# Kernel optimization log

Measured on AMD Instinct MI355X. Metric: run time of the kernel, lower is better.

## Reference

```python
import jax, jax.numpy as jnp
import numpy as np

B, SZ_C, S, D_KV, H_DIM = 2048, 8, 32, 32, 512
NEG = B // 4  # batchsize > 64 branch
TEMP = 0.5
EPS = 1e-8
BN_EPS = 1e-5


def setup_inputs() -> dict:
    key = jax.random.key(0)
    ks = jax.random.split(key, 8)
    x = jax.random.normal(ks[0], (B, SZ_C, S, D_KV), dtype=jnp.float32)
    W1 = jax.random.normal(ks[1], (H_DIM, D_KV), dtype=jnp.float32) * 0.05
    b1 = jnp.zeros((H_DIM,), jnp.float32)
    gamma = jnp.ones((H_DIM,), jnp.float32)
    beta = jnp.zeros((H_DIM,), jnp.float32)
    W2 = jax.random.normal(ks[2], (D_KV, H_DIM), dtype=jnp.float32) * 0.05
    b2 = jnp.zeros((D_KV,), jnp.float32)
    fcW = jax.random.normal(ks[3], (32, S * D_KV), dtype=jnp.float32) * 0.03
    fcb = jnp.zeros((32,), jnp.float32)
    # negatives: raw draws in [0, B-1); shifted past the self index inside reference
    neg_idx = jax.random.randint(ks[4], (B, NEG), 0, B - 1, dtype=jnp.int32)
    return {"x": x, "W1": W1, "b1": b1, "gamma": gamma, "beta": beta,
            "W2": W2, "b2": b2, "fcW": fcW, "fcb": fcb, "neg_idx": neg_idx}


def reference(x, W1, b1, gamma, beta, W2, b2, fcW, fcb, neg_idx):
    # per-channel MLP with training-mode BatchNorm (stats over the B*S rows of each channel)
    xc = jnp.transpose(x, (1, 0, 2, 3)).reshape(SZ_C, B * S, D_KV)   # [C, N, d_kv]
    h = jnp.einsum('cnd,hd->cnh', xc, W1) + b1                        # [C, N, h]
    mu = jnp.mean(h, axis=1, keepdims=True)
    var = jnp.mean((h - mu) ** 2, axis=1, keepdims=True)              # biased, as BN
    h = jax.nn.relu((h - mu) * jax.lax.rsqrt(var + BN_EPS) * gamma + beta)
    y = jnp.einsum('cnh,dh->cnd', h, W2) + b2                         # [C, N, d_kv]
    y = y.reshape(SZ_C, B, S * D_KV)                                  # raw flatten == torch views
    Zc = jnp.einsum('cbf,of->cbo', y, fcW) + fcb                      # [C, B, 32]
    Z = jnp.transpose(Zc, (1, 0, 2))                                  # [B, C, 32]

    Zn = Z / jnp.clip(jnp.linalg.norm(Z, axis=-1, keepdims=True), EPS, None)

    # shift raw draws in [0, B-1) past i -> uniform over indices != i
    idx = neg_idx + (neg_idx >= jnp.arange(B, dtype=neg_idx.dtype)[:, None]).astype(neg_idx.dtype)
    neg = Zn[idx]                                                     # [B, NEG, C, 32]
    neg_sim = jnp.einsum('bcd,bncd->bn', Zn, neg) / SZ_C              # mean over channels

    # mean pairwise cosine similarity across channels (j < k)
    G = jnp.einsum('bjd,bkd->bjk', Zn, Zn)                            # [B, C, C]
    mask = jnp.triu(jnp.ones((SZ_C, SZ_C), bool), 1)
    num_comb = SZ_C * (SZ_C - 1) // 2
    pos_sim = jnp.where(mask, G, 0.0).sum(axis=(1, 2)) / num_comb     # [B]

    l = jnp.exp(pos_sim / TEMP) / jnp.sum(jnp.exp(neg_sim / TEMP), axis=1)  # [B]
    Z_out = jnp.mean(Z, axis=1)                                       # [B, 32]
    return Z_out, l
```

## Files before the change

### kernel.cpp

```cpp
#include <hip/hip_runtime.h>
#include <hip/hip_bf16.h>
#include <math.h>

#define NB 2048
#define NC 8
#define NNEG 512

typedef __attribute__((ext_vector_type(8))) short bf16x8;
typedef __attribute__((ext_vector_type(4))) float f32x4;
typedef __attribute__((ext_vector_type(16))) float f32x16;

static __device__ __forceinline__ unsigned short f2b(float f) {
  __hip_bfloat16 h = __float2bfloat16(f);
  return *reinterpret_cast<unsigned short*>(&h);
}
static __device__ __forceinline__ unsigned int packbf2(float a, float b) {
  return (unsigned int)f2b(a) | ((unsigned int)f2b(b) << 16);
}

#define WS_SSUM   0
#define WS_SPROD  256
#define WS_B1EFF  8448
#define WS_Z      12544
#define WS_POS    536832
#define WS_W1B    538880
#define WS_W2B    604416
#define WS_FCWB   612608
#define WS_ZNB    628992

__global__ __launch_bounds__(256) void k_stats(const float* __restrict__ x,
                        float* __restrict__ Ssum, float* __restrict__ Sprod) {
  int c = blockIdx.y;
  int t = threadIdx.x;
  int w = t >> 6, l = t & 63;
  int col = l & 31, half = l >> 5;
  f32x16 acc;
  #pragma unroll
  for (int r = 0; r < 16; ++r) acc[r] = 0.f;
  float ssum = 0.f;
  #pragma unroll 2
  for (int i = 0; i < 8; ++i) {
    int chunk = blockIdx.x * 32 + i * 4 + w;
    int b = chunk >> 1;
    int sb = (chunk & 1) * 16 + half * 8;
    const float* base = x + ((size_t)(b * NC + c)) * 1024 + sb * 32 + col;
    float v0 = base[0],   v1 = base[32],  v2 = base[64],  v3 = base[96];
    float v4 = base[128], v5 = base[160], v6 = base[192], v7 = base[224];
    ssum += ((v0 + v1) + (v2 + v3)) + ((v4 + v5) + (v6 + v7));
    bf16x8 f;
    f[0] = (short)f2b(v0); f[1] = (short)f2b(v1);
    f[2] = (short)f2b(v2); f[3] = (short)f2b(v3);
    f[4] = (short)f2b(v4); f[5] = (short)f2b(v5);
    f[6] = (short)f2b(v6); f[7] = (short)f2b(v7);
    acc = __builtin_amdgcn_mfma_f32_32x32x16_bf16(f, f, acc, 0, 0, 0);
  }
  __shared__ float pr[4][1024];
  __shared__ float sred[4][32];
  #pragma unroll
  for (int r = 0; r < 16; ++r) {
    int row = (r & 3) + 8 * (r >> 2) + 4 * half;
    pr[w][row * 32 + col] = acc[r];
  }
  float sv = ssum + __shfl_xor(ssum, 32);
  if (l < 32) sred[w][l] = sv;
  __syncthreads();
  #pragma unroll
  for (int p = 0; p < 4; ++p) {
    int cell = t + p * 256;
    atomicAdd(&Sprod[c * 1024 + cell],
              (pr[0][cell] + pr[1][cell]) + (pr[2][cell] + pr[3][cell]));
  }
  if (t < 32)
    atomicAdd(&Ssum[c * 32 + t],
              (sred[0][t] + sred[1][t]) + (sred[2][t] + sred[3][t]));
}

__global__ void k_foldcvt(const float* __restrict__ W1, const float* __restrict__ b1,
                       const float* __restrict__ gamma, const float* __restrict__ beta,
                       const float* __restrict__ Ssum, const float* __restrict__ Sprod,
                       const float* __restrict__ W2, const float* __restrict__ fcW,
                       unsigned short* __restrict__ W1B, float* __restrict__ b1eff,
                       unsigned short* __restrict__ W2B, unsigned short* __restrict__ fcWB) {
  if (blockIdx.x >= 16) {
    int i = (blockIdx.x - 16) * 256 + threadIdx.x;
    if (i < 32 * 512) W2B[i] = f2b(W2[i]);
    fcWB[i] = f2b(fcW[i]);
    return;
  }
  int g = blockIdx.x * 256 + threadIdx.x;
  int c = g >> 9, h = g & 511;
  const float invN = 1.0f / (float)(NB * 32);
  float w[32];
  #pragma unroll
  for (int d = 0; d < 32; ++d) w[d] = W1[h * 32 + d];
  const float* M = Sprod + c * 1024;
  float q = 0.f;
  for (int j = 0; j < 32; ++j) {
    float v = 0.f;
    #pragma unroll
    for (int i2 = 0; i2 < 32; ++i2) v = fmaf(w[i2], M[i2 * 32 + j], v);
    q = fmaf(v, w[j], q);
  }
  float wmu = 0.f;
  #pragma unroll
  for (int d = 0; d < 32; ++d) wmu = fmaf(w[d], Ssum[c * 32 + d] * invN, wmu);
  float bb = b1[h];
  float mean = wmu + bb;
  float e2 = q * invN + 2.f * bb * wmu + bb * bb;
  float var = e2 - mean * mean;
  float alpha = gamma[h] * rsqrtf(var + 1e-5f);
  #pragma unroll
  for (int d = 0; d < 32; ++d)
    W1B[((size_t)c * 512 + h) * 32 + d] = f2b(w[d] * alpha);
  b1eff[c * 512 + h] = (bb - mean) * alpha + beta[h];
}

__global__ __launch_bounds__(256, 4) void k_main(
    const float* __restrict__ x, const unsigned short* __restrict__ W1B,
    const float* __restrict__ b1eff, const unsigned short* __restrict__ W2B,
    const float* __restrict__ b2, const unsigned short* __restrict__ fcWB,
    const float* __restrict__ fcb, float* __restrict__ Z) {
  int c = blockIdx.y;
  int bt = blockIdx.x;
  int t = threadIdx.x;
  int w = t >> 6, l = t & 63;
  int lr = l & 15, lg = l >> 4;

  __shared__ unsigned short buf[8 * 1280];
  __shared__ float zred[2][8][32];

  const unsigned short* W1c = W1B + (size_t)c * 512 * 32;
  const float* b1e = b1eff + c * 512;

  bf16x8 xf[4];
  #pragma unroll
  for (int sb = 0; sb < 4; ++sb) {
    int bl = 2 * w + (sb >> 1);
    int s = (sb & 1) * 16 + lr;
    const float* src = x + (((size_t)(bt * 8 + bl) * NC + c) * 32 + s) * 32 + lg * 8;
    float4 v0 = ((const float4*)src)[0];
    float4 v1 = ((const float4*)src)[1];
    bf16x8 p;
    p[0] = (short)f2b(v0.x); p[1] = (short)f2b(v0.y);
    p[2] = (short)f2b(v0.z); p[3] = (short)f2b(v0.w);
    p[4] = (short)f2b(v1.x); p[5] = (short)f2b(v1.y);
    p[6] = (short)f2b(v1.z); p[7] = (short)f2b(v1.w);
    xf[sb] = p;
  }

  f32x4 yacc[4][2];
  #pragma unroll
  for (int db = 0; db < 2; ++db) {
    f32x4 bv = *((const f32x4*)(b2 + db * 16 + lg * 4));
    #pragma unroll
    for (int mb = 0; mb < 4; ++mb) yacc[mb][db] = bv;
  }

  const f32x4 fzero = {0.f, 0.f, 0.f, 0.f};
  int row0 = 64 * w;

  for (int ch = 0; ch < 16; ++ch) {
    #pragma unroll
    for (int hb = 0; hb < 2; ++hb) {
      int h0 = ch * 32 + hb * 16;
      bf16x8 wf = *(const bf16x8*)&W1c[(size_t)(h0 + lr) * 32 + lg * 8];
      f32x4 bias = *((const f32x4*)(b1e + h0 + lg * 4));
      #pragma unroll
      for (int sb = 0; sb < 4; ++sb) {
        f32x4 d = __builtin_amdgcn_mfma_f32_16x16x32_bf16(wf, xf[sb], fzero, 0, 0, 0);
        float r0 = fmaxf(d[0] + bias[0], 0.f);
        float r1 = fmaxf(d[1] + bias[1], 0.f);
        float r2 = fmaxf(d[2] + bias[2], 0.f);
        float r3 = fmaxf(d[3] + bias[3], 0.f);
        uint2 pk; pk.x = packbf2(r0, r1); pk.y = packbf2(r2, r3);
        *(uint2*)&buf[(row0 + sb * 16 + lr) * 40 + hb * 16 + lg * 4] = pk;
      }
    }
    bf16x8 w20 = *(const bf16x8*)&W2B[(size_t)lr * 512 + ch * 32 + lg * 8];
    bf16x8 w21 = *(const bf16x8*)&W2B[(size_t)(16 + lr) * 512 + ch * 32 + lg * 8];
    #pragma unroll
    for (int mb = 0; mb < 4; ++mb) {
      bf16x8 hf = *(const bf16x8*)&buf[(row0 + mb * 16 + lr) * 40 + lg * 8];
      yacc[mb][0] = __builtin_amdgcn_mfma_f32_16x16x32_bf16(w20, hf, yacc[mb][0], 0, 0, 0);
      yacc[mb][1] = __builtin_amdgcn_mfma_f32_16x16x32_bf16(w21, hf, yacc[mb][1], 0, 0, 0);
    }
  }

  #pragma unroll
  for (int mb = 0; mb < 4; ++mb) {
    int bl = 2 * w + (mb >> 1);
    int s = (mb & 1) * 16 + lr;
    #pragma unroll
    for (int db = 0; db < 2; ++db) {
      uint2 pk;
      pk.x = packbf2(yacc[mb][db][0], yacc[mb][db][1]);
      pk.y = packbf2(yacc[mb][db][2], yacc[mb][db][3]);
      *(uint2*)&buf[bl * 1280 + s * 40 + db * 16 + lg * 4] = pk;
    }
  }
  __syncthreads();

  int nt = w & 1, kh = w >> 1;
  int arow = (lr < 8) ? lr : 7;
  f32x4 zacc = {0.f, 0.f, 0.f, 0.f};
  #pragma unroll
  for (int ks = 0; ks < 16; ++ks) {
    int s = kh * 16 + ks;
    bf16x8 afc = *(const bf16x8*)&buf[arow * 1280 + s * 40 + lg * 8];
    bf16x8 bfc = *(const bf16x8*)&fcWB[(size_t)(nt * 16 + lr) * 1024 + s * 32 + lg * 8];
    zacc = __builtin_amdgcn_mfma_f32_16x16x32_bf16(afc, bfc, zacc, 0, 0, 0);
  }
  if (lg < 2) {
    #pragma unroll
    for (int r = 0; r < 4; ++r) zred[kh][lg * 4 + r][nt * 16 + lr] = zacc[r];
  }
  __syncthreads();
  {
    int bloc = t >> 5, o = t & 31;
    Z[((size_t)(bt * 8 + bloc) * NC + c) * 32 + o] =
        zred[0][bloc][o] + zred[1][bloc][o] + fcb[o];
  }
}

__global__ void k_znorm(const float* __restrict__ Z, unsigned short* __restrict__ Znb,
                        float* __restrict__ possim, float* __restrict__ out) {
  int b = blockIdx.x;
  int t = threadIdx.x;
  float v = Z[(size_t)b * 256 + t];
  float n2 = v * v;
  #pragma unroll
  for (int m = 16; m >= 1; m >>= 1) n2 += __shfl_xor(n2, m, 64);
  float nrm = fmaxf(sqrtf(n2), 1e-8f);
  float zn = v / nrm;
  Znb[(size_t)b * 256 + t] = f2b(zn);
  __shared__ float sz[256];
  __shared__ float szn[256];
  sz[t] = v; szn[t] = zn;
  __syncthreads();
  if (t < 32) {
    float s = 0.f;
    #pragma unroll
    for (int cc = 0; cc < 8; ++cc) s += sz[cc * 32 + t];
    out[(size_t)b * 32 + t] = s * 0.125f;
    float sd = 0.f, t1 = 0.f;
    #pragma unroll
    for (int cc = 0; cc < 8; ++cc) {
      float z2 = szn[cc * 32 + t];
      sd += z2; t1 = fmaf(z2, z2, t1);
    }
    float t2 = sd * sd;
    #pragma unroll
    for (int m = 16; m >= 1; m >>= 1) {
      t2 += __shfl_xor(t2, m, 64);
      t1 += __shfl_xor(t1, m, 64);
    }
    if (t == 0) possim[b] = (t2 - t1) * 0.5f / 28.0f;
  }
}

__global__ __launch_bounds__(256) void k_negsim(
    const unsigned short* __restrict__ Znb, const int* __restrict__ neg_idx,
    const float* __restrict__ possim, float* __restrict__ lout) {
  int b = blockIdx.x;
  int t = threadIdx.x;
  int w = t >> 6, l = t & 63;
  int lr = l & 15, lg = l >> 4;
  __shared__ uint4 selfv[32];
  __shared__ float rs[4];
  if (t < 32) selfv[t] = ((const uint4*)(Znb + (size_t)b * 256))[t];
  __syncthreads();
  const unsigned short* selfp = (const unsigned short*)selfv;
  const f32x4 fzero = {0.f, 0.f, 0.f, 0.f};
  float esum = 0.f;
  #pragma unroll 2
  for (int mb = 0; mb < 8; ++mb) {
    int m0 = w * 128 + mb * 16;
    int raw = neg_idx[(size_t)b * NNEG + m0 + lr];
    int j = raw + (raw >= b ? 1 : 0);
    const unsigned short* rp = Znb + (size_t)j * 256;
    f32x4 acc = fzero;
    #pragma unroll
    for (int ks = 0; ks < 8; ++ks) {
      bf16x8 af = *(const bf16x8*)(rp + ks * 32 + lg * 8);
      bf16x8 bf = *(const bf16x8*)(selfp + ks * 32 + lg * 8);
      acc = __builtin_amdgcn_mfma_f32_16x16x32_bf16(af, bf, acc, 0, 0, 0);
    }
    if (lr == 0) {
      esum += expf(acc[0] * 0.25f) + expf(acc[1] * 0.25f)
            + expf(acc[2] * 0.25f) + expf(acc[3] * 0.25f);
    }
  }
  #pragma unroll
  for (int m = 32; m >= 1; m >>= 1) esum += __shfl_xor(esum, m, 64);
  if (l == 0) rs[w] = esum;
  __syncthreads();
  if (t == 0) {
    float tot = rs[0] + rs[1] + rs[2] + rs[3];
    lout[b] = expf(possim[b] * 2.0f) / tot;
  }
}

extern "C" void kernel_launch(void* const* d_in, const int* in_sizes, int n_in,
                              void* d_out, int out_size, void* d_ws, size_t ws_size,
                              hipStream_t stream) {
  const float* x     = (const float*)d_in[0];
  const float* W1    = (const float*)d_in[1];
  const float* b1    = (const float*)d_in[2];
  const float* gamma = (const float*)d_in[3];
  const float* beta  = (const float*)d_in[4];
  const float* W2    = (const float*)d_in[5];
  const float* b2    = (const float*)d_in[6];
  const float* fcW   = (const float*)d_in[7];
  const float* fcb   = (const float*)d_in[8];
  const int*   nidx  = (const int*)d_in[9];
  float* ws = (float*)d_ws;
  float* Ssum   = ws + WS_SSUM;
  float* Sprod  = ws + WS_SPROD;
  float* b1eff  = ws + WS_B1EFF;
  float* Z      = ws + WS_Z;
  float* possim = ws + WS_POS;
  unsigned short* W1Bp  = (unsigned short*)(ws + WS_W1B);
  unsigned short* W2Bp  = (unsigned short*)(ws + WS_W2B);
  unsigned short* fcWBp = (unsigned short*)(ws + WS_FCWB);
  unsigned short* Znbp  = (unsigned short*)(ws + WS_ZNB);
  float* out = (float*)d_out;

  hipMemsetAsync(ws, 0, (256 + 8192) * sizeof(float), stream);
  k_stats<<<dim3(128, 8), 256, 0, stream>>>(x, Ssum, Sprod);
  k_foldcvt<<<144, 256, 0, stream>>>(W1, b1, gamma, beta, Ssum, Sprod, W2, fcW,
                                     W1Bp, b1eff, W2Bp, fcWBp);
  k_main<<<dim3(256, 8), 256, 0, stream>>>(x, W1Bp, b1eff, W2Bp, b2, fcWBp, fcb, Z);
  k_znorm<<<NB, 256, 0, stream>>>(Z, Znbp, possim, out);
  k_negsim<<<NB, 256, 0, stream>>>(Znbp, nidx, possim, out + NB * 32);
}
```

Before: 178.6 us.

## Switch main MLP to 32x32x16 MFMA with register-resident hidden via permlane swap

Rewrites the per-channel two-layer MLP in k_main to use 32x32x16 bf16 MFMA tiles. The hidden activations now go straight from the first GEMM's accumulators into the second GEMM's operands through v_permlane32_swap, with no LDS round-trip. The b1 bias is folded into the accumulator init, and the y staging buffer uses an XOR-swizzled layout to reduce bank conflicts for the fc stage. The goal is to remove LDS traffic and the per-tile adds from the hidden layer, in exchange for more register pressure and reliance on a gfx950-specific instruction.

```diff
diff --git a/kernel.cpp b/kernel.cpp
--- a/kernel.cpp
+++ b/kernel.cpp
@@ -124,78 +124,90 @@
   int bt = blockIdx.x;
   int t = threadIdx.x;
   int w = t >> 6, l = t & 63;
+  int col = l & 31, half = l >> 5;
   int lr = l & 15, lg = l >> 4;
 
-  __shared__ unsigned short buf[8 * 1280];
+  __shared__ __align__(16) unsigned int ybf[8 * 520];
   __shared__ float zred[2][8][32];
 
   const unsigned short* W1c = W1B + (size_t)c * 512 * 32;
   const float* b1e = b1eff + c * 512;
 
-  bf16x8 xf[4];
-  #pragma unroll
-  for (int sb = 0; sb < 4; ++sb) {
-    int bl = 2 * w + (sb >> 1);
-    int s = (sb & 1) * 16 + lr;
-    const float* src = x + (((size_t)(bt * 8 + bl) * NC + c) * 32 + s) * 32 + lg * 8;
-    float4 v0 = ((const float4*)src)[0];
-    float4 v1 = ((const float4*)src)[1];
-    bf16x8 p;
-    p[0] = (short)f2b(v0.x); p[1] = (short)f2b(v0.y);
-    p[2] = (short)f2b(v0.z); p[3] = (short)f2b(v0.w);
-    p[4] = (short)f2b(v1.x); p[5] = (short)f2b(v1.y);
-    p[6] = (short)f2b(v1.z); p[7] = (short)f2b(v1.w);
-    xf[sb] = p;
-  }
-
-  f32x4 yacc[4][2];
-  #pragma unroll
-  for (int db = 0; db < 2; ++db) {
-    f32x4 bv = *((const f32x4*)(b2 + db * 16 + lg * 4));
-    #pragma unroll
-    for (int mb = 0; mb < 4; ++mb) yacc[mb][db] = bv;
-  }
-
-  const f32x4 fzero = {0.f, 0.f, 0.f, 0.f};
-  int row0 = 64 * w;
-
-  for (int ch = 0; ch < 16; ++ch) {
-    #pragma unroll
-    for (int hb = 0; hb < 2; ++hb) {
-      int h0 = ch * 32 + hb * 16;
-      bf16x8 wf = *(const bf16x8*)&W1c[(size_t)(h0 + lr) * 32 + lg * 8];
-      f32x4 bias = *((const f32x4*)(b1e + h0 + lg * 4));
+  bf16x8 xf[2][2];
+  #pragma unroll
+  for (int bi = 0; bi < 2; ++bi) {
+    int bg = bt * 8 + 2 * w + bi;
+    const float* xr = x + (((size_t)bg * NC + c) * 32 + col) * 32 + half * 8;
+    #pragma unroll
+    for (int kc = 0; kc < 2; ++kc) {
+      float4 v0 = ((const float4*)(xr + kc * 16))[0];
+      float4 v1 = ((const float4*)(xr + kc * 16))[1];
+      bf16x8 p;
+      p[0] = (short)f2b(v0.x); p[1] = (short)f2b(v0.y);
+      p[2] = (short)f2b(v0.z); p[3] = (short)f2b(v0.w);
+      p[4] = (short)f2b(v1.x); p[5] = (short)f2b(v1.y);
+      p[6] = (short)f2b(v1.z); p[7] = (short)f2b(v1.w);
+      xf[bi][kc] = p;
+    }
+  }
+
+  f32x16 yacc[2];
+  #pragma unroll
+  for (int q = 0; q < 4; ++q) {
+    f32x4 bv = *(const f32x4*)(b2 + 8 * q + 4 * half);
+    #pragma unroll
+    for (int i = 0; i < 4; ++i) { yacc[0][4 * q + i] = bv[i]; yacc[1][4 * q + i] = bv[i]; }
+  }
+
+  #pragma unroll 2
+  for (int hg = 0; hg < 16; ++hg) {
+    int h0 = hg * 32;
+    bf16x8 wA0 = *(const bf16x8*)&W1c[(size_t)(h0 + col) * 32 + half * 8];
+    bf16x8 wA1 = *(const bf16x8*)&W1c[(size_t)(h0 + col) * 32 + 16 + half * 8];
+    bf16x8 w2A0 = *(const bf16x8*)&W2B[(size_t)col * 512 + h0 + half * 8];
+    bf16x8 w2A1 = *(const bf16x8*)&W2B[(size_t)col * 512 + h0 + 16 + half * 8];
+    f32x16 cb;
+    #pragma unroll
+    for (int q = 0; q < 4; ++q) {
+      f32x4 bv = *(const f32x4*)(b1e + h0 + 8 * q + 4 * half);
+      cb[4 * q + 0] = bv[0]; cb[4 * q + 1] = bv[1];
+      cb[4 * q + 2] = bv[2]; cb[4 * q + 3] = bv[3];
+    }
+    #pragma unroll
+    for (int bi = 0; bi < 2; ++bi) {
+      f32x16 d = __builtin_amdgcn_mfma_f32_32x32x16_bf16(wA0, xf[bi][0], cb, 0, 0, 0);
+      d = __builtin_amdgcn_mfma_f32_32x32x16_bf16(wA1, xf[bi][1], d, 0, 0, 0);
+      unsigned int u[8];
       #pragma unroll
-      for (int sb = 0; sb < 4; ++sb) {
-        f32x4 d = __builtin_amdgcn_mfma_f32_16x16x32_bf16(wf, xf[sb], fzero, 0, 0, 0);
-        float r0 = fmaxf(d[0] + bias[0], 0.f);
-        float r1 = fmaxf(d[1] + bias[1], 0.f);
-        float r2 = fmaxf(d[2] + bias[2], 0.f);
-        float r3 = fmaxf(d[3] + bias[3], 0.f);
-        uint2 pk; pk.x = packbf2(r0, r1); pk.y = packbf2(r2, r3);
-        *(uint2*)&buf[(row0 + sb * 16 + lr) * 40 + hb * 16 + lg * 4] = pk;
-      }
-    }
-    bf16x8 w20 = *(const bf16x8*)&W2B[(size_t)lr * 512 + ch * 32 + lg * 8];
-    bf16x8 w21 = *(const bf16x8*)&W2B[(size_t)(16 + lr) * 512 + ch * 32 + lg * 8];
-    #pragma unroll
-    for (int mb = 0; mb < 4; ++mb) {
-      bf16x8 hf = *(const bf16x8*)&buf[(row0 + mb * 16 + lr) * 40 + lg * 8];
-      yacc[mb][0] = __builtin_amdgcn_mfma_f32_16x16x32_bf16(w20, hf, yacc[mb][0], 0, 0, 0);
-      yacc[mb][1] = __builtin_amdgcn_mfma_f32_16x16x32_bf16(w21, hf, yacc[mb][1], 0, 0, 0);
-    }
-  }
-
-  #pragma unroll
-  for (int mb = 0; mb < 4; ++mb) {
-    int bl = 2 * w + (mb >> 1);
-    int s = (mb & 1) * 16 + lr;
-    #pragma unroll
-    for (int db = 0; db < 2; ++db) {
-      uint2 pk;
-      pk.x = packbf2(yacc[mb][db][0], yacc[mb][db][1]);
-      pk.y = packbf2(yacc[mb][db][2], yacc[mb][db][3]);
-      *(uint2*)&buf[bl * 1280 + s * 40 + db * 16 + lg * 4] = pk;
+      for (int q = 0; q < 8; ++q)
+        u[q] = packbf2(fmaxf(d[2 * q], 0.f), fmaxf(d[2 * q + 1], 0.f));
+      asm("v_permlane32_swap_b32 %0, %1" : "+v"(u[0]), "+v"(u[2]));
+      asm("v_permlane32_swap_b32 %0, %1" : "+v"(u[1]), "+v"(u[3]));
+      asm("v_permlane32_swap_b32 %0, %1" : "+v"(u[4]), "+v"(u[6]));
+      asm("v_permlane32_swap_b32 %0, %1" : "+v"(u[5]), "+v"(u[7]));
+      uint4 q0; q0.x = u[0]; q0.y = u[1]; q0.z = u[2]; q0.w = u[3];
+      uint4 q1; q1.x = u[4]; q1.y = u[5]; q1.z = u[6]; q1.w = u[7];
+      bf16x8 f0 = __builtin_bit_cast(bf16x8, q0);
+      bf16x8 f1 = __builtin_bit_cast(bf16x8, q1);
+      yacc[bi] = __builtin_amdgcn_mfma_f32_32x32x16_bf16(w2A0, f0, yacc[bi], 0, 0, 0);
+      yacc[bi] = __builtin_amdgcn_mfma_f32_32x32x16_bf16(w2A1, f1, yacc[bi], 0, 0, 0);
+    }
+  }
+
+  #pragma unroll
+  for (int bi = 0; bi < 2; ++bi) {
+    int bl = 2 * w + bi;
+    unsigned int yu[8];
+    #pragma unroll
+    for (int q = 0; q < 8; ++q)
+      yu[q] = packbf2(yacc[bi][2 * q], yacc[bi][2 * q + 1]);
+    int sbase = bl * 520 + col * 16;
+    int swz = 4 * (col & 3);
+    #pragma unroll
+    for (int p = 0; p < 4; ++p) {
+      int dp = (4 * p + 2 * half) ^ swz;
+      uint2 val; val.x = yu[2 * p]; val.y = yu[2 * p + 1];
+      *(uint2*)&ybf[sbase + dp] = val;
     }
   }
   __syncthreads();
@@ -206,7 +218,9 @@
   #pragma unroll
   for (int ks = 0; ks < 16; ++ks) {
     int s = kh * 16 + ks;
-    bf16x8 afc = *(const bf16x8*)&buf[arow * 1280 + s * 40 + lg * 8];
+    int dw0 = (lg * 4) ^ (4 * (s & 3));
+    uint4 av = *(const uint4*)&ybf[arow * 520 + s * 16 + dw0];
+    bf16x8 afc = __builtin_bit_cast(bf16x8, av);
     bf16x8 bfc = *(const bf16x8*)&fcWB[(size_t)(nt * 16 + lr) * 1024 + s * 32 + lg * 8];
     zacc = __builtin_amdgcn_mfma_f32_16x16x32_bf16(afc, bfc, zacc, 0, 0, 0);
   }
```

New measurement: 187.5 us. 5.0% more time.

## Software-pipeline the two MLP GEMMs in k_main with register-prefetched weights

Applied to the files above, without the earlier changes.

Restructures the per-chunk loop in k_main so that GEMM1 for chunk ch overlaps GEMM2 for chunk ch-1. Next-chunk W1, bias and W2 fragments are prefetched into registers. The b1eff bias is folded into the MFMA accumulator init instead of being added after the MFMA. The shared buffer is reshaped to a per-wave uint layout of 20 words per row, and launch bounds drop from 4 to 3 waves per SIMD to give the extra live registers room. This costs some occupancy in exchange for hiding LDS and MFMA latency.

```diff
diff --git a/kernel.cpp b/kernel.cpp
--- a/kernel.cpp
+++ b/kernel.cpp
@@ -115,7 +115,7 @@
   b1eff[c * 512 + h] = (bb - mean) * alpha + beta[h];
 }
 
-__global__ __launch_bounds__(256, 4) void k_main(
+__global__ __launch_bounds__(256, 3) void k_main(
     const float* __restrict__ x, const unsigned short* __restrict__ W1B,
     const float* __restrict__ b1eff, const unsigned short* __restrict__ W2B,
     const float* __restrict__ b2, const unsigned short* __restrict__ fcWB,
@@ -126,11 +126,12 @@
   int w = t >> 6, l = t & 63;
   int lr = l & 15, lg = l >> 4;
 
-  __shared__ unsigned short buf[8 * 1280];
+  __shared__ unsigned int rbuf[4][64][20];
   __shared__ float zred[2][8][32];
 
   const unsigned short* W1c = W1B + (size_t)c * 512 * 32;
   const float* b1e = b1eff + c * 512;
+  unsigned int* rbw = &rbuf[w][0][0];
 
   bf16x8 xf[4];
   #pragma unroll
@@ -156,57 +157,87 @@
     for (int mb = 0; mb < 4; ++mb) yacc[mb][db] = bv;
   }
 
-  const f32x4 fzero = {0.f, 0.f, 0.f, 0.f};
-  int row0 = 64 * w;
-
-  for (int ch = 0; ch < 16; ++ch) {
-    #pragma unroll
-    for (int hb = 0; hb < 2; ++hb) {
-      int h0 = ch * 32 + hb * 16;
-      bf16x8 wf = *(const bf16x8*)&W1c[(size_t)(h0 + lr) * 32 + lg * 8];
-      f32x4 bias = *((const f32x4*)(b1e + h0 + lg * 4));
-      #pragma unroll
-      for (int sb = 0; sb < 4; ++sb) {
-        f32x4 d = __builtin_amdgcn_mfma_f32_16x16x32_bf16(wf, xf[sb], fzero, 0, 0, 0);
-        float r0 = fmaxf(d[0] + bias[0], 0.f);
-        float r1 = fmaxf(d[1] + bias[1], 0.f);
-        float r2 = fmaxf(d[2] + bias[2], 0.f);
-        float r3 = fmaxf(d[3] + bias[3], 0.f);
-        uint2 pk; pk.x = packbf2(r0, r1); pk.y = packbf2(r2, r3);
-        *(uint2*)&buf[(row0 + sb * 16 + lr) * 40 + hb * 16 + lg * 4] = pk;
-      }
-    }
-    bf16x8 w20 = *(const bf16x8*)&W2B[(size_t)lr * 512 + ch * 32 + lg * 8];
-    bf16x8 w21 = *(const bf16x8*)&W2B[(size_t)(16 + lr) * 512 + ch * 32 + lg * 8];
-    #pragma unroll
-    for (int mb = 0; mb < 4; ++mb) {
-      bf16x8 hf = *(const bf16x8*)&buf[(row0 + mb * 16 + lr) * 40 + lg * 8];
-      yacc[mb][0] = __builtin_amdgcn_mfma_f32_16x16x32_bf16(w20, hf, yacc[mb][0], 0, 0, 0);
-      yacc[mb][1] = __builtin_amdgcn_mfma_f32_16x16x32_bf16(w21, hf, yacc[mb][1], 0, 0, 0);
-    }
-  }
+  bf16x8 wfR[2];   f32x4 biasR[2];   bf16x8 w2fR[2];   bf16x8 hfreg[4];
+  wfR[0]  = *(const bf16x8*)&W1c[(size_t)lr * 32 + lg * 8];
+  wfR[1]  = *(const bf16x8*)&W1c[(size_t)(16 + lr) * 32 + lg * 8];
+  biasR[0] = *(const f32x4*)(b1e + lg * 4);
+  biasR[1] = *(const f32x4*)(b1e + 16 + lg * 4);
+
+#define GEMM1(dfr) \
+  _Pragma("unroll") for (int hb = 0; hb < 2; ++hb) \
+  _Pragma("unroll") for (int sb = 0; sb < 4; ++sb) \
+    dfr[hb][sb] = __builtin_amdgcn_mfma_f32_16x16x32_bf16(wfR[hb], xf[sb], biasR[hb], 0, 0, 0);
+
+#define GEMM2() \
+  _Pragma("unroll") for (int mb = 0; mb < 4; ++mb) { \
+    yacc[mb][0] = __builtin_amdgcn_mfma_f32_16x16x32_bf16(w2fR[0], hfreg[mb], yacc[mb][0], 0, 0, 0); \
+    yacc[mb][1] = __builtin_amdgcn_mfma_f32_16x16x32_bf16(w2fR[1], hfreg[mb], yacc[mb][1], 0, 0, 0); \
+  }
+
+#define PACKWRITE(dfr) \
+  _Pragma("unroll") for (int hb = 0; hb < 2; ++hb) \
+  _Pragma("unroll") for (int sb = 0; sb < 4; ++sb) { \
+    uint2 pk; \
+    pk.x = packbf2(fmaxf(dfr[hb][sb][0], 0.f), fmaxf(dfr[hb][sb][1], 0.f)); \
+    pk.y = packbf2(fmaxf(dfr[hb][sb][2], 0.f), fmaxf(dfr[hb][sb][3], 0.f)); \
+    *(uint2*)&rbw[(sb * 16 + lr) * 20 + hb * 8 + lg * 2] = pk; \
+  }
+
+#define LOADW(ch) { \
+    if ((ch) < 15) { \
+      int h1 = ((ch) + 1) * 32; \
+      wfR[0]  = *(const bf16x8*)&W1c[(size_t)(h1 + lr) * 32 + lg * 8]; \
+      wfR[1]  = *(const bf16x8*)&W1c[(size_t)(h1 + 16 + lr) * 32 + lg * 8]; \
+      biasR[0] = *(const f32x4*)(b1e + h1 + lg * 4); \
+      biasR[1] = *(const f32x4*)(b1e + h1 + 16 + lg * 4); \
+    } \
+    w2fR[0] = *(const bf16x8*)&W2B[(size_t)lr * 512 + (ch) * 32 + lg * 8]; \
+    w2fR[1] = *(const bf16x8*)&W2B[(size_t)(16 + lr) * 512 + (ch) * 32 + lg * 8]; \
+  }
+
+#define READH() \
+  _Pragma("unroll") for (int mb = 0; mb < 4; ++mb) \
+    hfreg[mb] = *(const bf16x8*)&rbw[(mb * 16 + lr) * 20 + lg * 4];
+
+  {
+    f32x4 dfr[2][4];
+    GEMM1(dfr);
+    PACKWRITE(dfr);
+    LOADW(0);
+    READH();
+  }
+  #pragma unroll 3
+  for (int ch = 1; ch < 16; ++ch) {
+    f32x4 dfr[2][4];
+    GEMM1(dfr);
+    GEMM2();
+    PACKWRITE(dfr);
+    LOADW(ch);
+    READH();
+  }
+  GEMM2();
 
   #pragma unroll
   for (int mb = 0; mb < 4; ++mb) {
-    int bl = 2 * w + (mb >> 1);
-    int s = (mb & 1) * 16 + lr;
     #pragma unroll
     for (int db = 0; db < 2; ++db) {
       uint2 pk;
       pk.x = packbf2(yacc[mb][db][0], yacc[mb][db][1]);
       pk.y = packbf2(yacc[mb][db][2], yacc[mb][db][3]);
-      *(uint2*)&buf[bl * 1280 + s * 40 + db * 16 + lg * 4] = pk;
+      *(uint2*)&rbw[(mb * 16 + lr) * 20 + db * 8 + lg * 2] = pk;
     }
   }
   __syncthreads();
 
   int nt = w & 1, kh = w >> 1;
   int arow = (lr < 8) ? lr : 7;
+  const unsigned int* ybase = &rbuf[arow >> 1][(arow & 1) * 32][0];
   f32x4 zacc = {0.f, 0.f, 0.f, 0.f};
   #pragma unroll
   for (int ks = 0; ks < 16; ++ks) {
     int s = kh * 16 + ks;
-    bf16x8 afc = *(const bf16x8*)&buf[arow * 1280 + s * 40 + lg * 8];
+    uint4 av = *(const uint4*)&ybase[s * 20 + lg * 4];
+    bf16x8 afc = __builtin_bit_cast(bf16x8, av);
     bf16x8 bfc = *(const bf16x8*)&fcWB[(size_t)(nt * 16 + lr) * 1024 + s * 32 + lg * 8];
     zacc = __builtin_amdgcn_mfma_f32_16x16x32_bf16(afc, bfc, zacc, 0, 0, 0);
   }
@@ -220,6 +251,11 @@
     Z[((size_t)(bt * 8 + bloc) * NC + c) * 32 + o] =
         zred[0][bloc][o] + zred[1][bloc][o] + fcb[o];
   }
+#undef GEMM1
+#undef GEMM2
+#undef PACKWRITE
+#undef LOADW
+#undef READH
 }
 
 __global__ void k_znorm(const float* __restrict__ Z, unsigned short* __restrict__ Znb,
```

Result: no change. 179.4 us (+0.4%).
